# Optimization experiments

Measured on AMD Instinct MI355X. Metric: run time of the kernel, lower is better.

Reference implementation:

```python
import jax, jax.numpy as jnp
import numpy as np

B, S, D, H, L = 4, 2048, 512, 8, 4
DFF = 4 * D
CW = 128          # context_window
LS_MIN, LS_MAX = -6.0, 1.5


def setup_inputs() -> dict:
    key = jax.random.key(0)
    ks = jax.random.split(key, 10)
    s = 0.02
    p = lambda k, shape: jax.random.normal(k, shape, jnp.float32) * s
    return {
        "x": jax.random.normal(ks[0], (B, S, 2), jnp.float32),
        "W_in": p(ks[1], (D, 2)), "b_in": jnp.zeros((D,), jnp.float32),
        "pos": p(ks[2], (1, S, D)),
        "Wqkv": p(ks[3], (L, 3 * D, D)), "bqkv": jnp.zeros((L, 3 * D), jnp.float32),
        "Wo": p(ks[4], (L, D, D)), "bo": jnp.zeros((L, D), jnp.float32),
        "W1": p(ks[5], (L, DFF, D)), "b1": jnp.zeros((L, DFF), jnp.float32),
        "W2": p(ks[6], (L, D, DFF)), "b2": jnp.zeros((L, D), jnp.float32),
        "ln1_g": jnp.ones((L, D), jnp.float32), "ln1_b": jnp.zeros((L, D), jnp.float32),
        "ln2_g": jnp.ones((L, D), jnp.float32), "ln2_b": jnp.zeros((L, D), jnp.float32),
        "W_head": p(ks[7], (4, D)), "b_head": jnp.zeros((4,), jnp.float32),
    }


def _ln(x, g, b):
    m = x.mean(-1, keepdims=True)
    v = ((x - m) ** 2).mean(-1, keepdims=True)
    return (x - m) / jnp.sqrt(v + 1e-5) * g + b


def reference(x, W_in, b_in, pos, Wqkv, bqkv, Wo, bo, W1, b1, W2, b2,
              ln1_g, ln1_b, ln2_g, ln2_b, W_head, b_head):
    Bx, Sx, _ = x.shape
    h = x @ W_in.T + b_in + pos[:, :Sx, :]          # [B,S,D]
    idx = jnp.arange(Sx)
    # True = disallowed: future OR older than context window
    mask = (idx[None, :] > idx[:, None]) | (idx[None, :] < idx[:, None] - CW)
    dh = D // H
    scale = 1.0 / np.sqrt(dh).astype(np.float32)
    neg = jnp.float32(-1e30)
    for l in range(L):
        # self-attention (post-LN, as nn.TransformerEncoderLayer default)
        qkv = h @ Wqkv[l].T + bqkv[l]               # [B,S,3D]
        q, k, v = jnp.split(qkv, 3, axis=-1)
        q = q.reshape(Bx, Sx, H, dh)
        k = k.reshape(Bx, Sx, H, dh)
        v = v.reshape(Bx, Sx, H, dh)
        scores = jnp.einsum('bqhd,bkhd->bhqk', q, k) * scale
        scores = jnp.where(mask, neg, scores)
        attn = jax.nn.softmax(scores, axis=-1)
        o = jnp.einsum('bhqk,bkhd->bqhd', attn, v).reshape(Bx, Sx, D)
        h = _ln(h + o @ Wo[l].T + bo[l], ln1_g[l], ln1_b[l])
        # GELU FFN (exact erf gelu, torch default)
        ff = jax.nn.gelu(h @ W1[l].T + b1[l], approximate=False) @ W2[l].T + b2[l]
        h = _ln(h + ff, ln2_g[l], ln2_b[l])
    out = h @ W_head.T + b_head                     # [B,S,4]
    mu = out[..., :2]
    log_sigma = jnp.clip(out[..., 2:], LS_MIN, LS_MAX)
    return mu, log_sigma
```

## Files before the change

### kernel.cpp

```cpp
#include <hip/hip_runtime.h>
#include <hip/hip_bf16.h>
#include <math.h>

constexpr int Bc = 4;
constexpr int Sc = 2048;
constexpr int Dc = 512;
constexpr int Hc = 8;
constexpr int DHc = 64;
constexpr int Lc = 4;
constexpr int DFFc = 2048;
constexpr int Tc = Bc * Sc;
constexpr int QKVW = 3 * Dc;

typedef __attribute__((ext_vector_type(8))) short short8;
typedef __attribute__((ext_vector_type(4))) float f32x4;
typedef __attribute__((ext_vector_type(4))) float float4v;
typedef __attribute__((ext_vector_type(4))) unsigned int uint4v;
typedef __attribute__((ext_vector_type(2))) unsigned int uint2v;

static __device__ __forceinline__ float u16tof(unsigned int u) {
  return __uint_as_float(u << 16);
}
static __device__ __forceinline__ unsigned short ftobf(float f) {
  __hip_bfloat16 h = __float2bfloat16(f);
  return *reinterpret_cast<unsigned short*>(&h);
}
static __device__ __forceinline__ void gload_lds16(const void* g, void* l) {
  __builtin_amdgcn_global_load_lds(
      (const __attribute__((address_space(1))) void*)g,
      (__attribute__((address_space(3))) void*)l, 16, 0, 0);
}

static __device__ __forceinline__ int swzK(int row, int col) {
  return row * 64 + ((((col >> 3) ^ (row & 7)) << 3) | (col & 7));
}
static __device__ __forceinline__ int swzW(int row, int col) {
  return row * 192 + ((((col >> 3) ^ (row & 7)) << 3) | (col & 7));
}
static __device__ __forceinline__ int gperm(int row, int ch) {
  return (row >> 1) * 8 + (((((row & 1) << 2) | ch)) ^ ((row >> 1) & 7));
}

__global__ __launch_bounds__(256) void k_f2bf4(const float* __restrict__ p0,
                                               const float* __restrict__ p1,
                                               const float* __restrict__ p2,
                                               const float* __restrict__ p3,
                                               unsigned short* __restrict__ o0,
                                               unsigned short* __restrict__ o1,
                                               unsigned short* __restrict__ o2,
                                               unsigned short* __restrict__ o3,
                                               int n0, int n01, int n012, int n0123) {
  int i4 = (blockIdx.x * 256 + threadIdx.x) * 4;
  if (i4 >= n0123) return;
  const float* src;
  unsigned short* dst;
  int off;
  if (i4 < n0) { src = p0; dst = o0; off = i4; }
  else if (i4 < n01) { src = p1; dst = o1; off = i4 - n0; }
  else if (i4 < n012) { src = p2; dst = o2; off = i4 - n01; }
  else { src = p3; dst = o3; off = i4 - n012; }
  float4v v = *(const float4v*)&src[off];
  uint2v pk = {ftobf(v[0]) | ((unsigned int)ftobf(v[1]) << 16),
               ftobf(v[2]) | ((unsigned int)ftobf(v[3]) << 16)};
  *(uint2v*)&dst[off] = pk;
}

__global__ __launch_bounds__(256) void k_embed(const float* __restrict__ x,
                                               const float* __restrict__ W_in,
                                               const float* __restrict__ b_in,
                                               const float* __restrict__ pos,
                                               float* __restrict__ h,
                                               unsigned short* __restrict__ hb) {
  int i4 = (blockIdx.x * 256 + threadIdx.x) * 4;
  int t = i4 >> 9;
  int d = i4 & 511;
  int s = t & (Sc - 1);
  float x0 = x[t * 2 + 0], x1 = x[t * 2 + 1];
  float4v w01 = *(const float4v*)&W_in[d * 2];
  float4v w23 = *(const float4v*)&W_in[d * 2 + 4];
  float4v pz = *(const float4v*)&pos[(size_t)s * Dc + d];
  float4v b4 = *(const float4v*)&b_in[d];
  float4v v;
  v[0] = x0 * w01[0] + x1 * w01[1] + b4[0] + pz[0];
  v[1] = x0 * w01[2] + x1 * w01[3] + b4[1] + pz[1];
  v[2] = x0 * w23[0] + x1 * w23[1] + b4[2] + pz[2];
  v[3] = x0 * w23[2] + x1 * w23[3] + b4[3] + pz[3];
  *(float4v*)&h[i4] = v;
  uint2v pk = {ftobf(v[0]) | ((unsigned int)ftobf(v[1]) << 16),
               ftobf(v[2]) | ((unsigned int)ftobf(v[3]) << 16)};
  *(uint2v*)&hb[i4] = pk;
}

template <int MODE, int OUTBF>
__global__ __launch_bounds__(256, 4) void k_mgemm2(const unsigned short* __restrict__ A,
                                                   const unsigned short* __restrict__ W,
                                                   const float* __restrict__ bias,
                                                   void* __restrict__ Cout,
                                                   int M, int N, int K) {
  __shared__ short SMEM[2][2][512 * 8];
  const int tid = threadIdx.x;
  const int lane = tid & 63;
  const int wid = tid >> 6;
  const int wm = wid >> 1;
  const int wn = wid & 1;

  const int nwg = gridDim.x * gridDim.y;
  const int bid = blockIdx.y * gridDim.x + blockIdx.x;
  const int swz = (bid & 7) * (nwg >> 3) + (bid >> 3);
  const int m0 = (swz / gridDim.x) * 128;
  const int n0 = (swz % gridDim.x) * 128;

  int r0S, c0S, r1S, c1S;
  {
    int p = tid;
    int rp = p >> 3, q = (p & 7) ^ (rp & 7);
    r0S = (rp << 1) | (q >> 2);
    c0S = q & 3;
    p = tid + 256;
    rp = p >> 3;
    q = (p & 7) ^ (rp & 7);
    r1S = (rp << 1) | (q >> 2);
    c1S = q & 3;
  }
  const unsigned short* a0p = A + (size_t)(m0 + r0S) * K + c0S * 8;
  const unsigned short* a1p = A + (size_t)(m0 + r1S) * K + c1S * 8;
  const unsigned short* b0p = W + (size_t)(n0 + r0S) * K + c0S * 8;
  const unsigned short* b1p = W + (size_t)(n0 + r1S) * K + c1S * 8;
  const int d0 = (tid & ~63) * 8;
  const int d1 = ((tid + 256) & ~63) * 8;

  f32x4 acc[4][4] = {};
  const int lr = lane & 15;
  const int chr = lane >> 4;

  gload_lds16(a0p, &SMEM[0][0][d0]);
  gload_lds16(a1p, &SMEM[0][0][d1]);
  gload_lds16(b0p, &SMEM[1][0][d0]);
  gload_lds16(b1p, &SMEM[1][0][d1]);
  __syncthreads();

  const int nsteps = K >> 5;
  int buf = 0;
  for (int s = 0; s < nsteps; ++s) {
    if (s + 1 < nsteps) {
      const int ko = (s + 1) << 5;
      gload_lds16(a0p + ko, &SMEM[0][buf ^ 1][d0]);
      gload_lds16(a1p + ko, &SMEM[0][buf ^ 1][d1]);
      gload_lds16(b0p + ko, &SMEM[1][buf ^ 1][d0]);
      gload_lds16(b1p + ko, &SMEM[1][buf ^ 1][d1]);
    }
    short8 af[4], bfr[4];
#pragma unroll
    for (int mi = 0; mi < 4; ++mi)
      af[mi] = *(const short8*)&SMEM[0][buf][gperm(wm * 64 + mi * 16 + lr, chr) * 8];
#pragma unroll
    for (int ni = 0; ni < 4; ++ni)
      bfr[ni] = *(const short8*)&SMEM[1][buf][gperm(wn * 64 + ni * 16 + lr, chr) * 8];
#pragma unroll
    for (int mi = 0; mi < 4; ++mi)
#pragma unroll
      for (int ni = 0; ni < 4; ++ni)
        acc[mi][ni] = __builtin_amdgcn_mfma_f32_16x16x32_bf16(
            af[mi], bfr[ni], acc[mi][ni], 0, 0, 0);
    __syncthreads();
    buf ^= 1;
  }

  float* cw = (float*)&SMEM[0][0][0] + wid * (16 * 68);
  const int cj = lane & 15;
  const int rj4 = (lane >> 4) * 4;
  const int rrd = lane >> 3;
  const int crd = (lane & 7) * 8;
#pragma unroll
  for (int mi = 0; mi < 4; ++mi) {
#pragma unroll
    for (int ni = 0; ni < 4; ++ni) {
      float bn = bias[n0 + wn * 64 + ni * 16 + cj];
#pragma unroll
      for (int j = 0; j < 4; ++j) {
        float v = acc[mi][ni][j] + bn;
        if (MODE == 2) v = 0.5f * v * (1.0f + erff(v * 0.70710678118654752f));
        cw[(rj4 + j) * 68 + ni * 16 + cj] = v;
      }
    }
    __builtin_amdgcn_sched_barrier(0);
#pragma unroll
    for (int t = 0; t < 2; ++t) {
      int rl = t * 8 + rrd;
      float4v v0 = *(const float4v*)&cw[rl * 68 + crd];
      float4v v1 = *(const float4v*)&cw[rl * 68 + crd + 4];
      size_t gbase = (size_t)(m0 + wm * 64 + mi * 16 + rl) * N +
                     (n0 + wn * 64 + crd);
      if (OUTBF) {
        unsigned int w0 = ftobf(v0[0]) | ((unsigned int)ftobf(v0[1]) << 16);
        unsigned int w1 = ftobf(v0[2]) | ((unsigned int)ftobf(v0[3]) << 16);
        unsigned int w2 = ftobf(v1[0]) | ((unsigned int)ftobf(v1[1]) << 16);
        unsigned int w3 = ftobf(v1[2]) | ((unsigned int)ftobf(v1[3]) << 16);
        uint4v pk = {w0, w1, w2, w3};
        *(uint4v*)&((unsigned short*)Cout)[gbase] = pk;
      } else {
        *(float4v*)&((float*)Cout)[gbase] = v0;
        *(float4v*)&((float*)Cout)[gbase + 4] = v1;
      }
    }
    __builtin_amdgcn_sched_barrier(0);
  }
}

template <int MODE, int OUTBF>
__global__ __launch_bounds__(256, 3) void k_mgemm3(const unsigned short* __restrict__ A,
                                                   const unsigned short* __restrict__ W,
                                                   const float* __restrict__ bias,
                                                   void* __restrict__ Cout,
                                                   int M, int N, int K) {
  __shared__ short SMEM[3][2][512 * 8];
  const int tid = threadIdx.x;
  const int lane = tid & 63;
  const int wid = tid >> 6;
  const int wm = wid >> 1;
  const int wn = wid & 1;

  const int nwg = gridDim.x * gridDim.y;
  const int bid = blockIdx.y * gridDim.x + blockIdx.x;
  const int swz = (bid & 7) * (nwg >> 3) + (bid >> 3);
  const int m0 = (swz / gridDim.x) * 128;
  const int n0 = (swz % gridDim.x) * 128;

  int r0S, c0S, r1S, c1S;
  {
    int p = tid;
    int rp = p >> 3, q = (p & 7) ^ (rp & 7);
    r0S = (rp << 1) | (q >> 2);
    c0S = q & 3;
    p = tid + 256;
    rp = p >> 3;
    q = (p & 7) ^ (rp & 7);
    r1S = (rp << 1) | (q >> 2);
    c1S = q & 3;
  }
  const unsigned short* a0p = A + (size_t)(m0 + r0S) * K + c0S * 8;
  const unsigned short* a1p = A + (size_t)(m0 + r1S) * K + c1S * 8;
  const unsigned short* b0p = W + (size_t)(n0 + r0S) * K + c0S * 8;
  const unsigned short* b1p = W + (size_t)(n0 + r1S) * K + c1S * 8;
  const int d0 = (tid & ~63) * 8;
  const int d1 = ((tid + 256) & ~63) * 8;

  f32x4 acc[4][4] = {};
  const int lr = lane & 15;
  const int chr = lane >> 4;

#pragma unroll
  for (int t = 0; t < 2; ++t) {
    const int ko = t << 5;
    gload_lds16(a0p + ko, &SMEM[t][0][d0]);
    gload_lds16(a1p + ko, &SMEM[t][0][d1]);
    gload_lds16(b0p + ko, &SMEM[t][1][d0]);
    gload_lds16(b1p + ko, &SMEM[t][1][d1]);
  }

  const int nsteps = K >> 5;
  for (int s = 0; s < nsteps; ++s) {
    if (s + 1 < nsteps)
      asm volatile("s_waitcnt vmcnt(4)" ::: "memory");
    else
      asm volatile("s_waitcnt vmcnt(0)" ::: "memory");
    __builtin_amdgcn_s_barrier();
    __builtin_amdgcn_sched_barrier(0);

    if (s + 2 < nsteps) {
      const int ko = (s + 2) << 5;
      const int nb = (s + 2) % 3;
      gload_lds16(a0p + ko, &SMEM[nb][0][d0]);
      gload_lds16(a1p + ko, &SMEM[nb][0][d1]);
      gload_lds16(b0p + ko, &SMEM[nb][1][d0]);
      gload_lds16(b1p + ko, &SMEM[nb][1][d1]);
    }

    const int buf = s % 3;
    short8 af[4], bfr[4];
#pragma unroll
    for (int mi = 0; mi < 4; ++mi)
      af[mi] = *(const short8*)&SMEM[buf][0][gperm(wm * 64 + mi * 16 + lr, chr) * 8];
#pragma unroll
    for (int ni = 0; ni < 4; ++ni)
      bfr[ni] = *(const short8*)&SMEM[buf][1][gperm(wn * 64 + ni * 16 + lr, chr) * 8];
    asm volatile("s_waitcnt lgkmcnt(0)" ::: "memory");
    __builtin_amdgcn_sched_barrier(0);
#pragma unroll
    for (int mi = 0; mi < 4; ++mi)
#pragma unroll
      for (int ni = 0; ni < 4; ++ni)
        acc[mi][ni] = __builtin_amdgcn_mfma_f32_16x16x32_bf16(
            af[mi], bfr[ni], acc[mi][ni], 0, 0, 0);
  }
  __syncthreads();

  float* cw = (float*)&SMEM[0][0][0] + wid * (16 * 68);
  const int cj = lane & 15;
  const int rj4 = (lane >> 4) * 4;
  const int rrd = lane >> 3;
  const int crd = (lane & 7) * 8;
#pragma unroll
  for (int mi = 0; mi < 4; ++mi) {
#pragma unroll
    for (int ni = 0; ni < 4; ++ni) {
      float bn = bias[n0 + wn * 64 + ni * 16 + cj];
#pragma unroll
      for (int j = 0; j < 4; ++j) {
        float v = acc[mi][ni][j] + bn;
        if (MODE == 2) v = 0.5f * v * (1.0f + erff(v * 0.70710678118654752f));
        cw[(rj4 + j) * 68 + ni * 16 + cj] = v;
      }
    }
    __builtin_amdgcn_sched_barrier(0);
#pragma unroll
    for (int t = 0; t < 2; ++t) {
      int rl = t * 8 + rrd;
      float4v v0 = *(const float4v*)&cw[rl * 68 + crd];
      float4v v1 = *(const float4v*)&cw[rl * 68 + crd + 4];
      size_t gbase = (size_t)(m0 + wm * 64 + mi * 16 + rl) * N +
                     (n0 + wn * 64 + crd);
      if (OUTBF) {
        unsigned int w0 = ftobf(v0[0]) | ((unsigned int)ftobf(v0[1]) << 16);
        unsigned int w1 = ftobf(v0[2]) | ((unsigned int)ftobf(v0[3]) << 16);
        unsigned int w2 = ftobf(v1[0]) | ((unsigned int)ftobf(v1[1]) << 16);
        unsigned int w3 = ftobf(v1[2]) | ((unsigned int)ftobf(v1[3]) << 16);
        uint4v pk = {w0, w1, w2, w3};
        *(uint4v*)&((unsigned short*)Cout)[gbase] = pk;
      } else {
        *(float4v*)&((float*)Cout)[gbase] = v0;
        *(float4v*)&((float*)Cout)[gbase + 4] = v1;
      }
    }
    __builtin_amdgcn_sched_barrier(0);
  }
}

__global__ __launch_bounds__(256, 3) void k_attn(const unsigned short* __restrict__ qkv,
                                                 unsigned short* __restrict__ o) {
  __shared__ unsigned short KPs[192 * 64];
  __shared__ unsigned short Vt[64 * 192];

  const int tid = threadIdx.x;
  const int lane = tid & 63;
  const int w = tid >> 6;
  const int idx = blockIdx.x;
  const int qb = idx & 31;
  const int hh = (idx >> 5) & 7;
  const int b = idx >> 8;
  const int q0 = qb * 64;
  const int kstart = max(0, q0 - 128);
  const int nk = q0 + 64 - kstart;

  {
    const unsigned short* kbase = qkv + (size_t)(b * Sc + kstart) * QKVW + Dc + hh * DHc;
    const int ng = nk * 8;
    for (int c = tid; c < ng; c += 256) {
      int row = c >> 3, slot = c & 7;
      int sch = slot ^ (row & 7);
      gload_lds16(kbase + (size_t)row * QKVW + sch * 8,
                  (char*)KPs + (c & ~63) * 16);
    }
  }
  for (int c = tid; c < (nk >> 1) * 8; c += 256) {
    int jp = c >> 3, ch = c & 7;
    int j = jp * 2;
    const unsigned short* base =
        &qkv[(size_t)(b * Sc + kstart + j) * QKVW + 2 * Dc + hh * DHc + ch * 8];
    short8 v0 = *(const short8*)base;
    short8 v1 = *(const short8*)(base + QKVW);
#pragma unroll
    for (int i = 0; i < 8; ++i) {
      unsigned int pk = (unsigned short)v0[i] | ((unsigned int)(unsigned short)v1[i] << 16);
      *(unsigned int*)&Vt[swzW(ch * 8 + i, j)] = pk;
    }
  }
  if (nk < 192) {
    for (int c = tid; c < 64 * 64; c += 256) {
      int d = c >> 6, jo = c & 63;
      *(unsigned int*)&Vt[swzW(d, 64 + jo * 2)] = 0;
    }
  }

  const int qg = q0 + w * 16 + (lane & 15);
  const int kg8 = (lane >> 4) * 8;
  const unsigned short* qp = &qkv[(size_t)(b * Sc + qg) * QKVW + hh * DHc + kg8];
  short8 bq0 = *(const short8*)qp;
  short8 bq1 = *(const short8*)(qp + 32);
  __syncthreads();

  const int jb = max(0, q0 + w * 16 - 128) - kstart;

  f32x4 sacc[9];
#pragma unroll
  for (int t = 0; t < 9; ++t) {
    int key = jb + t * 16 + (lane & 15);
    short8 a0 = *(const short8*)&KPs[swzK(key, kg8)];
    short8 a1 = *(const short8*)&KPs[swzK(key, 32 + kg8)];
    f32x4 z = {0.f, 0.f, 0.f, 0.f};
    z = __builtin_amdgcn_mfma_f32_16x16x32_bf16(a0, bq0, z, 0, 0, 0);
    sacc[t] = __builtin_amdgcn_mfma_f32_16x16x32_bf16(a1, bq1, z, 0, 0, 0);
  }

  const int rj = (lane >> 4) * 4;
  float mx = -1e30f;
#pragma unroll
  for (int t = 0; t < 9; ++t) {
#pragma unroll
    for (int j = 0; j < 4; ++j) {
      int kglob = kstart + jb + t * 16 + rj + j;
      bool valid = (kglob <= qg) && (kglob + 128 >= qg);
      float s = valid ? sacc[t][j] * 0.125f : -1e30f;
      sacc[t][j] = s;
      mx = fmaxf(mx, s);
    }
  }
  mx = fmaxf(mx, __shfl_xor(mx, 16));
  mx = fmaxf(mx, __shfl_xor(mx, 32));
  float sum = 0.f;
#pragma unroll
  for (int t = 0; t < 9; ++t)
#pragma unroll
    for (int j = 0; j < 4; ++j) {
      float e = __expf(sacc[t][j] - mx);
      sacc[t][j] = e;
      sum += e;
    }
  sum += __shfl_xor(sum, 16);
  sum += __shfl_xor(sum, 32);
  const float inv = 1.0f / sum;

  __syncthreads();

  const int prow = w * 16 + (lane & 15);
#pragma unroll
  for (int t = 0; t < 9; ++t) {
    int c0 = jb + t * 16 + rj;
    unsigned int p0 = ftobf(sacc[t][0] * inv) |
                      ((unsigned int)ftobf(sacc[t][1] * inv) << 16);
    unsigned int p1 = ftobf(sacc[t][2] * inv) |
                      ((unsigned int)ftobf(sacc[t][3] * inv) << 16);
    *(unsigned int*)&KPs[swzW(prow, c0)] = p0;
    *(unsigned int*)&KPs[swzW(prow, c0 + 2)] = p1;
  }
  {
    int g2 = (lane >> 4) * 2;
    for (int col = g2; col < jb; col += 8)
      *(unsigned int*)&KPs[swzW(prow, col)] = 0;
    for (int col = jb + 144 + g2; col < 192; col += 8)
      *(unsigned int*)&KPs[swzW(prow, col)] = 0;
  }
  const int kb0 = jb >> 5;
  const int kbend = min(6, (jb + 144 + 31) >> 5);
  f32x4 oacc[4] = {};
  for (int kb = kb0; kb < kbend; ++kb) {
    short8 pa = *(const short8*)&KPs[swzW(prow, kb * 32 + kg8)];
#pragma unroll
    for (int dt = 0; dt < 4; ++dt) {
      short8 vb = *(const short8*)&Vt[swzW(dt * 16 + (lane & 15), kb * 32 + kg8)];
      oacc[dt] = __builtin_amdgcn_mfma_f32_16x16x32_bf16(pa, vb, oacc[dt], 0, 0, 0);
    }
  }
  const int cj = lane & 15;
#pragma unroll
  for (int j = 0; j < 4; ++j)
#pragma unroll
    for (int dt = 0; dt < 4; ++dt)
      o[(size_t)(b * Sc + q0 + w * 16 + rj + j) * Dc + hh * DHc + dt * 16 + cj] =
          ftobf(oacc[dt][j]);
}

__global__ __launch_bounds__(256) void k_lnr(float* __restrict__ h,
                                             const float* __restrict__ raw,
                                             const float* __restrict__ g,
                                             const float* __restrict__ bta,
                                             unsigned short* __restrict__ outb) {
  const int wid = threadIdx.x >> 6;
  const int lane = threadIdx.x & 63;
  const int t = blockIdx.x * 4 + wid;
  const float4v* hrow = (const float4v*)(h + (size_t)t * Dc);
  const float4v* rrow = (const float4v*)(raw + (size_t)t * Dc);
  float4v v[2];
  float sum = 0.0f, sq = 0.0f;
#pragma unroll
  for (int i = 0; i < 2; ++i) {
    float4v hv = hrow[lane + i * 64];
    float4v rv = rrow[lane + i * 64];
#pragma unroll
    for (int c = 0; c < 4; ++c) {
      float xv = rv[c] + hv[c];
      v[i][c] = xv;
      sum += xv;
      sq += xv * xv;
    }
  }
#pragma unroll
  for (int off = 32; off; off >>= 1) {
    sum += __shfl_xor(sum, off);
    sq += __shfl_xor(sq, off);
  }
  float m = sum * (1.0f / 512.0f);
  float var = sq * (1.0f / 512.0f) - m * m;
  float rstd = rsqrtf(var + 1e-5f);
  float4v* orow = (float4v*)(h + (size_t)t * Dc);
  unsigned int* brow = (unsigned int*)(outb + (size_t)t * Dc);
#pragma unroll
  for (int i = 0; i < 2; ++i) {
    int d4 = (lane + i * 64) * 4;
    float4v ov;
#pragma unroll
    for (int c = 0; c < 4; ++c)
      ov[c] = (v[i][c] - m) * rstd * g[d4 + c] + bta[d4 + c];
    orow[lane + i * 64] = ov;
    unsigned int p0 = ftobf(ov[0]) | ((unsigned int)ftobf(ov[1]) << 16);
    unsigned int p1 = ftobf(ov[2]) | ((unsigned int)ftobf(ov[3]) << 16);
    brow[(lane + i * 64) * 2] = p0;
    brow[(lane + i * 64) * 2 + 1] = p1;
  }
}

__global__ __launch_bounds__(256) void k_head(const float* __restrict__ h,
                                              const float* __restrict__ Wh,
                                              const float* __restrict__ bh,
                                              float* __restrict__ outp) {
  const int wid = threadIdx.x >> 6;
  const int lane = threadIdx.x & 63;
  const int t = blockIdx.x * 4 + wid;
  const float4v* row4 = (const float4v*)(h + (size_t)t * Dc);
  const float4v* w0r = (const float4v*)(Wh + 0 * Dc);
  const float4v* w1r = (const float4v*)(Wh + 1 * Dc);
  const float4v* w2r = (const float4v*)(Wh + 2 * Dc);
  const float4v* w3r = (const float4v*)(Wh + 3 * Dc);
  float a0 = 0, a1 = 0, a2 = 0, a3 = 0;
#pragma unroll
  for (int i = 0; i < 2; ++i) {
    int d4 = lane + i * 64;
    float4v xv = row4[d4];
    float4v v0 = w0r[d4];
    float4v v1 = w1r[d4];
    float4v v2 = w2r[d4];
    float4v v3 = w3r[d4];
#pragma unroll
    for (int c = 0; c < 4; ++c) {
      a0 += xv[c] * v0[c];
      a1 += xv[c] * v1[c];
      a2 += xv[c] * v2[c];
      a3 += xv[c] * v3[c];
    }
  }
#pragma unroll
  for (int off = 32; off; off >>= 1) {
    a0 += __shfl_xor(a0, off);
    a1 += __shfl_xor(a1, off);
    a2 += __shfl_xor(a2, off);
    a3 += __shfl_xor(a3, off);
  }
  if (lane == 0) {
    outp[(size_t)t * 2 + 0] = a0 + bh[0];
    outp[(size_t)t * 2 + 1] = a1 + bh[1];
    outp[(size_t)Tc * 2 + (size_t)t * 2 + 0] = fminf(fmaxf(a2 + bh[2], -6.0f), 1.5f);
    outp[(size_t)Tc * 2 + (size_t)t * 2 + 1] = fminf(fmaxf(a3 + bh[3], -6.0f), 1.5f);
  }
}

extern "C" void kernel_launch(void* const* d_in, const int* in_sizes, int n_in,
                              void* d_out, int out_size, void* d_ws, size_t ws_size,
                              hipStream_t stream) {
  const float* x    = (const float*)d_in[0];
  const float* W_in = (const float*)d_in[1];
  const float* b_in = (const float*)d_in[2];
  const float* pos  = (const float*)d_in[3];
  const float* Wqkv = (const float*)d_in[4];
  const float* bqkv = (const float*)d_in[5];
  const float* Wo   = (const float*)d_in[6];
  const float* bo   = (const float*)d_in[7];
  const float* W1   = (const float*)d_in[8];
  const float* b1   = (const float*)d_in[9];
  const float* W2   = (const float*)d_in[10];
  const float* b2   = (const float*)d_in[11];
  const float* ln1g = (const float*)d_in[12];
  const float* ln1b = (const float*)d_in[13];
  const float* ln2g = (const float*)d_in[14];
  const float* ln2b = (const float*)d_in[15];
  const float* Wh   = (const float*)d_in[16];
  const float* bh   = (const float*)d_in[17];
  float* out = (float*)d_out;

  char* p = (char*)d_ws;
  float* h   = (float*)p;          p += (size_t)Tc * Dc * 4;
  float* t2  = (float*)p;          p += (size_t)Tc * Dc * 4;
  unsigned short* hb  = (unsigned short*)p; p += (size_t)Tc * Dc * 2;
  unsigned short* ob  = (unsigned short*)p; p += (size_t)Tc * Dc * 2;
  unsigned short* big = (unsigned short*)p; p += (size_t)Tc * DFFc * 2;
  unsigned short* wqb = (unsigned short*)p; p += (size_t)Lc * QKVW * Dc * 2;
  unsigned short* wob = (unsigned short*)p; p += (size_t)Lc * Dc * Dc * 2;
  unsigned short* w1b = (unsigned short*)p; p += (size_t)Lc * DFFc * Dc * 2;
  unsigned short* w2b = (unsigned short*)p; p += (size_t)Lc * Dc * DFFc * 2;

  const int nq = Lc * QKVW * Dc;
  const int no = Lc * Dc * Dc;
  const int n1 = Lc * DFFc * Dc;
  const int n2 = Lc * Dc * DFFc;
  const int ntot = nq + no + n1 + n2;
  k_f2bf4<<<ntot / 1024, 256, 0, stream>>>(Wqkv, Wo, W1, W2, wqb, wob, w1b, w2b,
                                           nq, nq + no, nq + no + n1, ntot);

  k_embed<<<(Tc * Dc) / 1024, 256, 0, stream>>>(x, W_in, b_in, pos, h, hb);

  for (int l = 0; l < Lc; ++l) {
    const unsigned short* wq_l = wqb + (size_t)l * QKVW * Dc;
    const unsigned short* wo_l = wob + (size_t)l * Dc * Dc;
    const unsigned short* w1_l = w1b + (size_t)l * DFFc * Dc;
    const unsigned short* w2_l = w2b + (size_t)l * Dc * DFFc;

    k_mgemm3<0, 1><<<dim3(QKVW / 128, Tc / 128), 256, 0, stream>>>(
        hb, wq_l, bqkv + (size_t)l * QKVW, big, Tc, QKVW, Dc);

    k_attn<<<Bc * Hc * (Sc / 64), 256, 0, stream>>>(big, ob);

    k_mgemm3<0, 0><<<dim3(Dc / 128, Tc / 128), 256, 0, stream>>>(
        ob, wo_l, bo + (size_t)l * Dc, t2, Tc, Dc, Dc);

    k_lnr<<<Tc / 4, 256, 0, stream>>>(h, t2, ln1g + (size_t)l * Dc,
                                      ln1b + (size_t)l * Dc, hb);

    k_mgemm2<2, 1><<<dim3(DFFc / 128, Tc / 128), 256, 0, stream>>>(
        hb, w1_l, b1 + (size_t)l * DFFc, big, Tc, DFFc, Dc);

    k_mgemm3<0, 0><<<dim3(Dc / 128, Tc / 128), 256, 0, stream>>>(
        big, w2_l, b2 + (size_t)l * Dc, t2, Tc, Dc, DFFc);

    k_lnr<<<Tc / 4, 256, 0, stream>>>(h, t2, ln2g + (size_t)l * Dc,
                                      ln2b + (size_t)l * Dc, hb);
  }

  k_head<<<Tc / 4, 256, 0, stream>>>(h, Wh, bh, out);
}
```

Baseline: 558.5 us.

## Split the FFN down-projection GEMM over K and fuse partial sums into LayerNorm

Adds a split-K variant of the W2 GEMM that launches two K-halves as separate grid z-slices, each writing fp32 partials to its own buffer. A new LayerNorm kernel sums both partials with the residual before normalising. The aim is to double the workgroup count for this narrow-N GEMM, whose 256 tiles give roughly one workgroup per CU, so more waves are available to hide latency. The cost is an extra fp32 activation buffer written and read per layer. The path runs only when the workspace is large enough, otherwise it falls back to the original kernels.

```diff
diff --git a/kernel.cpp b/kernel.cpp
--- a/kernel.cpp
+++ b/kernel.cpp
@@ -336,6 +336,126 @@
   }
 }
 
+__global__ __launch_bounds__(256, 3) void k_mg3sk(const unsigned short* __restrict__ A,
+                                                  const unsigned short* __restrict__ W,
+                                                  const float* __restrict__ bias,
+                                                  float* __restrict__ P0,
+                                                  float* __restrict__ P1,
+                                                  int M, int N, int K) {
+  __shared__ short SMEM[3][2][512 * 8];
+  const int tid = threadIdx.x;
+  const int lane = tid & 63;
+  const int wid = tid >> 6;
+  const int wm = wid >> 1;
+  const int wn = wid & 1;
+  const int z = blockIdx.z;
+  const int koff = z * (K >> 1);
+
+  const int nwg = gridDim.x * gridDim.y;
+  const int bid = blockIdx.y * gridDim.x + blockIdx.x;
+  const int swz = (bid & 7) * (nwg >> 3) + (bid >> 3);
+  const int m0 = (swz / gridDim.x) * 128;
+  const int n0 = (swz % gridDim.x) * 128;
+
+  int r0S, c0S, r1S, c1S;
+  {
+    int p = tid;
+    int rp = p >> 3, q = (p & 7) ^ (rp & 7);
+    r0S = (rp << 1) | (q >> 2);
+    c0S = q & 3;
+    p = tid + 256;
+    rp = p >> 3;
+    q = (p & 7) ^ (rp & 7);
+    r1S = (rp << 1) | (q >> 2);
+    c1S = q & 3;
+  }
+  const unsigned short* a0p = A + (size_t)(m0 + r0S) * K + koff + c0S * 8;
+  const unsigned short* a1p = A + (size_t)(m0 + r1S) * K + koff + c1S * 8;
+  const unsigned short* b0p = W + (size_t)(n0 + r0S) * K + koff + c0S * 8;
+  const unsigned short* b1p = W + (size_t)(n0 + r1S) * K + koff + c1S * 8;
+  const int d0 = (tid & ~63) * 8;
+  const int d1 = ((tid + 256) & ~63) * 8;
+
+  f32x4 acc[4][4] = {};
+  const int lr = lane & 15;
+  const int chr = lane >> 4;
+
+#pragma unroll
+  for (int t = 0; t < 2; ++t) {
+    const int ko = t << 5;
+    gload_lds16(a0p + ko, &SMEM[t][0][d0]);
+    gload_lds16(a1p + ko, &SMEM[t][0][d1]);
+    gload_lds16(b0p + ko, &SMEM[t][1][d0]);
+    gload_lds16(b1p + ko, &SMEM[t][1][d1]);
+  }
+
+  const int nsteps = K >> 6;
+  for (int s = 0; s < nsteps; ++s) {
+    if (s + 1 < nsteps)
+      asm volatile("s_waitcnt vmcnt(4)" ::: "memory");
+    else
+      asm volatile("s_waitcnt vmcnt(0)" ::: "memory");
+    __builtin_amdgcn_s_barrier();
+    __builtin_amdgcn_sched_barrier(0);
+
+    if (s + 2 < nsteps) {
+      const int ko = (s + 2) << 5;
+      const int nb = (s + 2) % 3;
+      gload_lds16(a0p + ko, &SMEM[nb][0][d0]);
+      gload_lds16(a1p + ko, &SMEM[nb][0][d1]);
+      gload_lds16(b0p + ko, &SMEM[nb][1][d0]);
+      gload_lds16(b1p + ko, &SMEM[nb][1][d1]);
+    }
+
+    const int buf = s % 3;
+    short8 af[4], bfr[4];
+#pragma unroll
+    for (int mi = 0; mi < 4; ++mi)
+      af[mi] = *(const short8*)&SMEM[buf][0][gperm(wm * 64 + mi * 16 + lr, chr) * 8];
+#pragma unroll
+    for (int ni = 0; ni < 4; ++ni)
+      bfr[ni] = *(const short8*)&SMEM[buf][1][gperm(wn * 64 + ni * 16 + lr, chr) * 8];
+    asm volatile("s_waitcnt lgkmcnt(0)" ::: "memory");
+    __builtin_amdgcn_sched_barrier(0);
+#pragma unroll
+    for (int mi = 0; mi < 4; ++mi)
+#pragma unroll
+      for (int ni = 0; ni < 4; ++ni)
+        acc[mi][ni] = __builtin_amdgcn_mfma_f32_16x16x32_bf16(
+            af[mi], bfr[ni], acc[mi][ni], 0, 0, 0);
+  }
+  __syncthreads();
+
+  float* Cout = z ? P1 : P0;
+  float* cw = (float*)&SMEM[0][0][0] + wid * (16 * 68);
+  const int cj = lane & 15;
+  const int rj4 = (lane >> 4) * 4;
+  const int rrd = lane >> 3;
+  const int crd = (lane & 7) * 8;
+#pragma unroll
+  for (int mi = 0; mi < 4; ++mi) {
+#pragma unroll
+    for (int ni = 0; ni < 4; ++ni) {
+      float bn = z ? 0.0f : bias[n0 + wn * 64 + ni * 16 + cj];
+#pragma unroll
+      for (int j = 0; j < 4; ++j)
+        cw[(rj4 + j) * 68 + ni * 16 + cj] = acc[mi][ni][j] + bn;
+    }
+    __builtin_amdgcn_sched_barrier(0);
+#pragma unroll
+    for (int t = 0; t < 2; ++t) {
+      int rl = t * 8 + rrd;
+      float4v v0 = *(const float4v*)&cw[rl * 68 + crd];
+      float4v v1 = *(const float4v*)&cw[rl * 68 + crd + 4];
+      size_t gbase = (size_t)(m0 + wm * 64 + mi * 16 + rl) * N +
+                     (n0 + wn * 64 + crd);
+      *(float4v*)&Cout[gbase] = v0;
+      *(float4v*)&Cout[gbase + 4] = v1;
+    }
+    __builtin_amdgcn_sched_barrier(0);
+  }
+}
+
 __global__ __launch_bounds__(256, 3) void k_attn(const unsigned short* __restrict__ qkv,
                                                  unsigned short* __restrict__ o) {
   __shared__ unsigned short KPs[192 * 64];
@@ -489,6 +609,58 @@
 #pragma unroll
     for (int c = 0; c < 4; ++c) {
       float xv = rv[c] + hv[c];
+      v[i][c] = xv;
+      sum += xv;
+      sq += xv * xv;
+    }
+  }
+#pragma unroll
+  for (int off = 32; off; off >>= 1) {
+    sum += __shfl_xor(sum, off);
+    sq += __shfl_xor(sq, off);
+  }
+  float m = sum * (1.0f / 512.0f);
+  float var = sq * (1.0f / 512.0f) - m * m;
+  float rstd = rsqrtf(var + 1e-5f);
+  float4v* orow = (float4v*)(h + (size_t)t * Dc);
+  unsigned int* brow = (unsigned int*)(outb + (size_t)t * Dc);
+#pragma unroll
+  for (int i = 0; i < 2; ++i) {
+    int d4 = (lane + i * 64) * 4;
+    float4v ov;
+#pragma unroll
+    for (int c = 0; c < 4; ++c)
+      ov[c] = (v[i][c] - m) * rstd * g[d4 + c] + bta[d4 + c];
+    orow[lane + i * 64] = ov;
+    unsigned int p0 = ftobf(ov[0]) | ((unsigned int)ftobf(ov[1]) << 16);
+    unsigned int p1 = ftobf(ov[2]) | ((unsigned int)ftobf(ov[3]) << 16);
+    brow[(lane + i * 64) * 2] = p0;
+    brow[(lane + i * 64) * 2 + 1] = p1;
+  }
+}
+
+__global__ __launch_bounds__(256) void k_lnr2(float* __restrict__ h,
+                                              const float* __restrict__ raw0,
+                                              const float* __restrict__ raw1,
+                                              const float* __restrict__ g,
+                                              const float* __restrict__ bta,
+                                              unsigned short* __restrict__ outb) {
+  const int wid = threadIdx.x >> 6;
+  const int lane = threadIdx.x & 63;
+  const int t = blockIdx.x * 4 + wid;
+  const float4v* hrow = (const float4v*)(h + (size_t)t * Dc);
+  const float4v* r0row = (const float4v*)(raw0 + (size_t)t * Dc);
+  const float4v* r1row = (const float4v*)(raw1 + (size_t)t * Dc);
+  float4v v[2];
+  float sum = 0.0f, sq = 0.0f;
+#pragma unroll
+  for (int i = 0; i < 2; ++i) {
+    float4v hv = hrow[lane + i * 64];
+    float4v r0 = r0row[lane + i * 64];
+    float4v r1 = r1row[lane + i * 64];
+#pragma unroll
+    for (int c = 0; c < 4; ++c) {
+      float xv = (r0[c] + r1[c]) + hv[c];
       v[i][c] = xv;
       sum += xv;
       sq += xv * xv;
@@ -596,6 +768,9 @@
   unsigned short* wob = (unsigned short*)p; p += (size_t)Lc * Dc * Dc * 2;
   unsigned short* w1b = (unsigned short*)p; p += (size_t)Lc * DFFc * Dc * 2;
   unsigned short* w2b = (unsigned short*)p; p += (size_t)Lc * Dc * DFFc * 2;
+  float* t3 = (float*)p;
+  const size_t ws_needed = (size_t)(p - (char*)d_ws) + (size_t)Tc * Dc * 4;
+  const bool use_sk = (ws_size >= ws_needed);
 
   const int nq = Lc * QKVW * Dc;
   const int no = Lc * Dc * Dc;
@@ -627,11 +802,17 @@
     k_mgemm2<2, 1><<<dim3(DFFc / 128, Tc / 128), 256, 0, stream>>>(
         hb, w1_l, b1 + (size_t)l * DFFc, big, Tc, DFFc, Dc);
 
-    k_mgemm3<0, 0><<<dim3(Dc / 128, Tc / 128), 256, 0, stream>>>(
-        big, w2_l, b2 + (size_t)l * Dc, t2, Tc, Dc, DFFc);
-
-    k_lnr<<<Tc / 4, 256, 0, stream>>>(h, t2, ln2g + (size_t)l * Dc,
-                                      ln2b + (size_t)l * Dc, hb);
+    if (use_sk) {
+      k_mg3sk<<<dim3(Dc / 128, Tc / 128, 2), 256, 0, stream>>>(
+          big, w2_l, b2 + (size_t)l * Dc, t2, t3, Tc, Dc, DFFc);
+      k_lnr2<<<Tc / 4, 256, 0, stream>>>(h, t2, t3, ln2g + (size_t)l * Dc,
+                                         ln2b + (size_t)l * Dc, hb);
+    } else {
+      k_mgemm3<0, 0><<<dim3(Dc / 128, Tc / 128), 256, 0, stream>>>(
+          big, w2_l, b2 + (size_t)l * Dc, t2, Tc, Dc, DFFc);
+      k_lnr<<<Tc / 4, 256, 0, stream>>>(h, t2, ln2g + (size_t)l * Dc,
+                                        ln2b + (size_t)l * Dc, hb);
+    }
   }
 
   k_head<<<Tc / 4, 256, 0, stream>>>(h, Wh, bh, out);
```

Result: no change. 562.7 us (+0.8%).
